# Kernel optimization log

Hardware: AMD Instinct MI355X
Metric: run time of the kernel (lower is better)

## Reference

```python
import jax, jax.numpy as jnp
import numpy as np
import math

H = 1024
E = 16
ENT_STRENGTH = 0.5
COHERENCE_TIME = 10.0
TIME_STEP = 0.0
K = 2
# static list of rotation pairs (i<j), applied sequentially as in the torch double loop
PAIRS = np.array([(i, j) for i in range(E) for j in range(i + 1, E)], dtype=np.int32)


def _mlp(x, w1, b1, w2, b2):
    h = jax.nn.gelu(x @ w1 + b1, approximate=False)  # torch default GELU = exact erf
    return h @ w2 + b2


def _apply_entanglement(amps, ent):
    # sequential Givens rotations over expert pairs; carry shape [B,S,E]
    pairs = jnp.asarray(PAIRS)

    def step(carry, pair):
        i, j = pair[0], pair[1]
        angle = ent[i, j] * ENT_STRENGTH
        c, s = jnp.cos(angle), jnp.sin(angle)
        ai = jnp.take(carry, i, axis=-1)  # [B,S]
        aj = jnp.take(carry, j, axis=-1)
        oh_i = jax.nn.one_hot(i, E, dtype=carry.dtype)
        oh_j = jax.nn.one_hot(j, E, dtype=carry.dtype)
        new = (carry * (1.0 - oh_i - oh_j)
               + (c * ai - s * aj)[..., None] * oh_i
               + (s * ai + c * aj)[..., None] * oh_j)
        return new, None

    out, _ = jax.lax.scan(step, amps, pairs)
    return out


def setup_inputs() -> dict:
    key = jax.random.key(0)
    ks = jax.random.split(key, 10)
    sc1 = 1.0 / math.sqrt(H)
    sc2 = 1.0 / math.sqrt(H // 2)
    return {
        "hidden_states": jax.random.normal(ks[0], (4, 4096, H), dtype=jnp.float32),
        "w1a": jax.random.uniform(ks[1], (H, H // 2), jnp.float32, -sc1, sc1),
        "b1a": jnp.zeros((H // 2,), jnp.float32),
        "w2a": jax.random.uniform(ks[2], (H // 2, E), jnp.float32, -sc2, sc2),
        "b2a": jnp.zeros((E,), jnp.float32),
        "w1p": jax.random.uniform(ks[3], (H, H // 2), jnp.float32, -sc1, sc1),
        "b1p": jnp.zeros((H // 2,), jnp.float32),
        "w2p": jax.random.uniform(ks[4], (H // 2, E), jnp.float32, -sc2, sc2),
        "b2p": jnp.zeros((E,), jnp.float32),
        "ent": jax.random.normal(ks[5], (E, E), dtype=jnp.float32) * 0.1,
    }


def reference(hidden_states, w1a, b1a, w2a, b2a, w1p, b1p, w2p, b2p, ent):
    raw_amps = _mlp(hidden_states, w1a, b1a, w2a, b2a)                 # [B,S,E]
    raw_phases = jnp.tanh(_mlp(hidden_states, w1p, b1p, w2p, b2p)) * jnp.float32(math.pi)
    amplitudes = jnp.sqrt(jax.nn.softmax(jnp.abs(raw_amps), axis=-1))
    entangled = _apply_entanglement(amplitudes, ent)
    coherence = jnp.exp(jnp.float32(-TIME_STEP / COHERENCE_TIME))      # time_step buffer = 0 -> 1.0
    decoherent = entangled * coherence
    probs = decoherent ** 2
    probs = probs / jnp.maximum(jnp.sum(jnp.abs(probs), axis=-1, keepdims=True), 1e-12)
    top_p, top_i = jax.lax.top_k(probs, K)
    top_p = top_p / jnp.maximum(jnp.sum(jnp.abs(top_p), axis=-1, keepdims=True), 1e-12)
    return top_p, top_i, decoherent, raw_phases, probs
```

## Files before the change

kernel.cpp:

```cpp
#include <hip/hip_runtime.h>
#include <math.h>

#define NTOK   16384
#define HDIM   1024
#define HHALF  512
#define NE     16

#define OFF_TP  0
#define OFF_TI  (NTOK * 2)
#define OFF_DEC (NTOK * 4)
#define OFF_PH  (OFF_DEC + NTOK * NE)
#define OFF_PR  (OFF_PH + NTOK * NE)

typedef _Float16 half8 __attribute__((ext_vector_type(8)));
typedef _Float16 half4 __attribute__((ext_vector_type(4)));
typedef float f32x16 __attribute__((ext_vector_type(16)));
typedef float f32x4 __attribute__((ext_vector_type(4)));

#define LO_SCALE     2048.0f
#define LO_SCALE_INV (1.0f / 2048.0f)
#define MFMA32(a,b,c) __builtin_amdgcn_mfma_f32_32x32x16_f16(a,b,c,0,0,0)
#define MFMA16(a,b,c) __builtin_amdgcn_mfma_f32_16x16x32_f16(a,b,c,0,0,0)

__device__ __forceinline__ float gelu_exact(float x) {
    return 0.5f * x * (1.0f + erff(x * 0.70710678118654752440f));
}

__device__ __forceinline__ void cvt_split(float4 v, half4& hi, half4& lo) {
    _Float16 h0 = (_Float16)v.x, h1 = (_Float16)v.y,
             h2 = (_Float16)v.z, h3 = (_Float16)v.w;
    hi = (half4){h0, h1, h2, h3};
    lo = (half4){(_Float16)((v.x - (float)h0) * LO_SCALE),
                 (_Float16)((v.y - (float)h1) * LO_SCALE),
                 (_Float16)((v.z - (float)h2) * LO_SCALE),
                 (_Float16)((v.w - (float)h3) * LO_SCALE)};
}

__global__ void __launch_bounds__(256)
qir_wtrans(const float* __restrict__ w1a, const float* __restrict__ w1p,
           _Float16* __restrict__ wt, float* __restrict__ out)
{
    int u = blockIdx.x * 256 + threadIdx.x;
    out[OFF_PH + u] = 0.0f;
    out[OFF_PH + 262144 + u] = 0.0f;

    int l  = u & 63;
    int f  = (u >> 6) & 7;
    int sl = (u >> 9) & 7;
    int kc = (u >> 12) & 31;
    int ph = u >> 17;
    int nf = f >> 2, kh = (f >> 1) & 1, pl = f & 1;
    int col = sl * 64 + nf * 32 + (l & 31);
    int k0  = kc * 32 + kh * 16 + (l >> 5) * 8;
    const float* __restrict__ W = ph ? w1p : w1a;
    half8 v;
    #pragma unroll
    for (int j = 0; j < 8; ++j) {
        float x = W[(size_t)(k0 + j) * HHALF + col];
        _Float16 h = (_Float16)x;
        v[j] = pl ? (_Float16)((x - (float)h) * LO_SCALE) : h;
    }
    *(half8*)&wt[(size_t)u * 8] = v;
}

__device__ __forceinline__ void kstep(
    int kc, const float* __restrict__ aptr, const _Float16* __restrict__ bptr,
    char* Acur, char* Anxt, int a_rd, int a_off0, int a_off1,
    half8 (&Bc)[8], half8 (&Bn)[8],
    float4 (&xw)[2], float4 (&xl)[2],
    f32x16& a00, f32x16& a01, f32x16& a10, f32x16& a11,
    f32x16& c00, f32x16& c01, f32x16& c10, f32x16& c11)
{
    if (kc + 2 < 32) {
        xl[0] = *(const float4*)(aptr + (kc + 2) * 32);
        xl[1] = *(const float4*)(aptr + (kc + 2) * 32 + 16);
    }
    if (kc + 1 < 32) {
        #pragma unroll
        for (int f = 0; f < 8; ++f)
            Bn[f] = *(const half8*)(bptr + (size_t)(kc + 1) * 32768 + f * 512);
    }
    #pragma unroll
    for (int kh = 0; kh < 2; ++kh) {
        const char* Ah = Acur + kh * 4096 + a_rd;
        half8 ah0 = *(const half8*)(Ah);
        half8 ah1 = *(const half8*)(Ah + 512);
        half8 al0 = *(const half8*)(Ah + 8192);
        half8 al1 = *(const half8*)(Ah + 8192 + 512);
        half8 bh0 = Bc[kh * 2],     bl0 = Bc[kh * 2 + 1];
        half8 bh1 = Bc[4 + kh * 2], bl1 = Bc[4 + kh * 2 + 1];
        a00 = MFMA32(ah0, bh0, a00); c00 = MFMA32(al0, bh0, c00); c00 = MFMA32(ah0, bl0, c00);
        a01 = MFMA32(ah0, bh1, a01); c01 = MFMA32(al0, bh1, c01); c01 = MFMA32(ah0, bl1, c01);
        a10 = MFMA32(ah1, bh0, a10); c10 = MFMA32(al1, bh0, c10); c10 = MFMA32(ah1, bl0, c10);
        a11 = MFMA32(ah1, bh1, a11); c11 = MFMA32(al1, bh1, c11); c11 = MFMA32(ah1, bl1, c11);
    }
    if (kc + 1 < 32) {
        half4 hv, lv;
        cvt_split(xw[0], hv, lv);
        *(half4*)(Anxt + a_off0) = hv; *(half4*)(Anxt + a_off0 + 8192) = lv;
        cvt_split(xw[1], hv, lv);
        *(half4*)(Anxt + a_off1) = hv; *(half4*)(Anxt + a_off1 + 8192) = lv;
    }
    __syncthreads();
}

__global__ void __launch_bounds__(512, 2)
qir_gemm(const float* __restrict__ xg, const _Float16* __restrict__ wt,
         const float* __restrict__ b1a, const float* __restrict__ w2a, const float* __restrict__ b2a,
         const float* __restrict__ b1p, const float* __restrict__ w2p, const float* __restrict__ b2p,
         float* __restrict__ out)
{
    extern __shared__ char smem[];
    const int tid = threadIdx.x;
    const int l  = tid & 63;
    const int w  = tid >> 6;
    const int wm = w >> 2;
    const int wn = w & 3;
    const int bid  = blockIdx.x;
    const int ph   = bid & 1;
    const int nh   = (bid >> 1) & 1;
    const int mblk = bid >> 2;
    const int tok0 = mblk * 128;

    const float* __restrict__ b1 = ph ? b1p : b1a;
    const float* __restrict__ w2 = ph ? w2p : w2a;
    const float* __restrict__ b2 = ph ? b2p : b2a;
    const _Float16* __restrict__ wtp = wt + ((size_t)ph << 20);

    char* const Ab0 = smem;
    char* const Ab1 = smem + 16384;

    const int r  = tid >> 2;
    const int kq = tid & 3;
    const float* __restrict__ aptr = xg + (size_t)(tok0 + r) * HDIM + kq * 4;
    const int a_off0 = (kq >> 1) * 2048 + r * 16 + (kq & 1) * 8;
    const int a_off1 = a_off0 + 4096;
    const int a_rd = (l >> 5) * 2048 + (wm * 64 + (l & 31)) * 16;

    const _Float16* __restrict__ bptr = wtp + (nh * 4 + wn) * 4096 + (size_t)l * 8;

    f32x16 a00{}, a01{}, a10{}, a11{}, c00{}, c01{}, c10{}, c11{};
    #pragma unroll
    for (int rg = 0; rg < 16; ++rg) {
        a00[rg] = 0.f; a01[rg] = 0.f; a10[rg] = 0.f; a11[rg] = 0.f;
        c00[rg] = 0.f; c01[rg] = 0.f; c10[rg] = 0.f; c11[rg] = 0.f;
    }

    half8 Bc[8], Bn[8];
    float4 xw[2], xl[2];

    {
        float4 v0 = *(const float4*)(aptr);
        float4 v1 = *(const float4*)(aptr + 16);
        half4 hv, lv;
        cvt_split(v0, hv, lv);
        *(half4*)(Ab0 + a_off0) = hv; *(half4*)(Ab0 + a_off0 + 8192) = lv;
        cvt_split(v1, hv, lv);
        *(half4*)(Ab0 + a_off1) = hv; *(half4*)(Ab0 + a_off1 + 8192) = lv;
    }
    #pragma unroll
    for (int f = 0; f < 8; ++f) Bc[f] = *(const half8*)(bptr + f * 512);
    xw[0] = *(const float4*)(aptr + 32);
    xw[1] = *(const float4*)(aptr + 48);
    __syncthreads();

    for (int kk = 0; kk < 16; ++kk) {
        kstep(2 * kk,     aptr, bptr, Ab0, Ab1, a_rd, a_off0, a_off1,
              Bc, Bn, xw, xl, a00, a01, a10, a11, c00, c01, c10, c11);
        kstep(2 * kk + 1, aptr, bptr, Ab1, Ab0, a_rd, a_off0, a_off1,
              Bn, Bc, xl, xw, a00, a01, a10, a11, c00, c01, c10, c11);
    }

    const int col0 = nh * 256 + wn * 64 + (l & 31);
    const float bb0 = b1[col0], bb1 = b1[col0 + 32];
    #pragma unroll
    for (int rg = 0; rg < 16; ++rg) {
        a00[rg] = gelu_exact(a00[rg] + c00[rg] * LO_SCALE_INV + bb0);
        a01[rg] = gelu_exact(a01[rg] + c01[rg] * LO_SCALE_INV + bb1);
        a10[rg] = gelu_exact(a10[rg] + c10[rg] * LO_SCALE_INV + bb0);
        a11[rg] = gelu_exact(a11[rg] + c11[rg] * LO_SCALE_INV + bb1);
    }

    char* const Hw = smem + w * 4096;
    char* const hb = Hw + ((l >> 3) & 3) * 1024 + (l & 7) * 2;
    float* const P = (float*)(smem + 32768);

    half8 w2h[2], w2l[2];
    #pragma unroll
    for (int nf = 0; nf < 2; ++nf) {
        #pragma unroll
        for (int j = 0; j < 8; ++j) {
            int kg = nh * 256 + wn * 64 + nf * 32 + (l >> 4) * 8 + j;
            float v = w2[(size_t)kg * NE + (l & 15)];
            _Float16 hh = (_Float16)v;
            w2h[nf][j] = hh;
            w2l[nf][j] = (_Float16)((v - (float)hh) * LO_SCALE);
        }
    }

    f32x4 acc2[4], acc2s[4];
    #pragma unroll
    for (int m16 = 0; m16 < 4; ++m16)
        #pragma unroll
        for (int rg = 0; rg < 4; ++rg) { acc2[m16][rg] = 0.f; acc2s[m16][rg] = 0.f; }

#define H2PASS(ACC0, ACC1, NF, PL)                                             \
    {                                                                          \
        _Pragma("unroll")                                                      \
        for (int rg = 0; rg < 16; ++rg) {                                      \
            int row0 = (rg & 3) + 8 * (rg >> 2) + 4 * (l >> 5);                \
            { float vv = ACC0[rg]; _Float16 hh = (_Float16)vv;                 \
              *(_Float16*)(hb + row0 * 16) =                                   \
                  (PL) ? (_Float16)(vv - (float)hh) : hh; }                    \
            { float vv = ACC1[rg]; _Float16 hh = (_Float16)vv;                 \
              *(_Float16*)(hb + (32 + row0) * 16) =                            \
                  (PL) ? (_Float16)(vv - (float)hh) : hh; }                    \
        }                                                                      \
        _Pragma("unroll")                                                      \
        for (int m16 = 0; m16 < 4; ++m16) {                                    \
            half8 a2 = *(const half8*)(Hw + (l >> 4) * 1024 +                  \
                                       (m16 * 16 + (l & 15)) * 16);            \
            acc2[m16] = MFMA16(a2, w2h[NF], acc2[m16]);                        \
            if (!(PL)) acc2s[m16] = MFMA16(a2, w2l[NF], acc2s[m16]);           \
        }                                                                      \
    }

    H2PASS(a00, a10, 0, 0)
    H2PASS(a01, a11, 1, 0)
    H2PASS(a00, a10, 0, 1)
    H2PASS(a01, a11, 1, 1)
#undef H2PASS

    #pragma unroll
    for (int m16 = 0; m16 < 4; ++m16)
        #pragma unroll
        for (int rg = 0; rg < 4; ++rg) {
            int row = m16 * 16 + ((l >> 4) << 2) + rg;
            P[w * 1024 + row * 16 + (l & 15)] =
                acc2[m16][rg] + acc2s[m16][rg] * LO_SCALE_INV;
        }
    __syncthreads();

    #pragma unroll
    for (int rep = 0; rep < 4; ++rep) {
        int oi = tid + rep * 512;
        int t = oi >> 4, e = oi & 15;
        int bw = (t >> 6) * 4, tl = t & 63;
        float sum = 0.5f * b2[e]
                  + P[(bw + 0) * 1024 + tl * 16 + e]
                  + P[(bw + 1) * 1024 + tl * 16 + e]
                  + P[(bw + 2) * 1024 + tl * 16 + e]
                  + P[(bw + 3) * 1024 + tl * 16 + e];
        atomicAdd(out + (ph ? OFF_PH : OFF_PR) + (size_t)(tok0 + t) * NE + e, sum);
    }
}

__global__ void __launch_bounds__(512)
qir_mlp(const float* __restrict__ xg,
        const float* __restrict__ w1a, const float* __restrict__ b1a,
        const float* __restrict__ w2a, const float* __restrict__ b2a,
        const float* __restrict__ w1p, const float* __restrict__ b1p,
        const float* __restrict__ w2p, const float* __restrict__ b2p,
        float* __restrict__ out)
{
    __shared__ float sh_w[16][HHALF];
    __shared__ float sh_x[16][68];

    const int tid  = threadIdx.x;
    const int cg   = tid & 63;
    const int tg   = tid >> 6;
    const int tok0 = blockIdx.x * 64;
    const int cA   = cg * 4;
    const int cB   = 256 + cg * 4;

    for (int phase = 0; phase < 2; ++phase) {
        const float* __restrict__ w1 = phase ? w1p : w1a;
        const float* __restrict__ b1 = phase ? b1p : b1a;
        const float* __restrict__ w2 = phase ? w2p : w2a;
        const float* __restrict__ b2 = phase ? b2p : b2a;

        float acc[8][8];
        #pragma unroll
        for (int t = 0; t < 8; ++t)
            #pragma unroll
            for (int c = 0; c < 8; ++c) acc[t][c] = 0.0f;

        float4 wreg[4];
        float4 xreg = make_float4(0.f, 0.f, 0.f, 0.f);

        auto load_chunk = [&](int kc) {
            #pragma unroll
            for (int p = 0; p < 4; ++p) {
                int f  = tid + p * 512;
                int k  = f >> 7;
                int c4 = (f & 127) << 2;
                wreg[p] = *(const float4*)&w1[(kc * 16 + k) * HHALF + c4];
            }
            if (tid < 256) {
                int t  = tid >> 2;
                int k4 = (tid & 3) << 2;
                xreg = *(const float4*)&xg[(size_t)(tok0 + t) * HDIM + kc * 16 + k4];
            }
        };

        load_chunk(0);
        for (int kc = 0; kc < HDIM / 16; ++kc) {
            __syncthreads();
            #pragma unroll
            for (int p = 0; p < 4; ++p) {
                int f  = tid + p * 512;
                int k  = f >> 7;
                int c4 = (f & 127) << 2;
                *(float4*)&sh_w[k][c4] = wreg[p];
            }
            if (tid < 256) {
                int t  = tid >> 2;
                int k4 = (tid & 3) << 2;
                sh_x[k4 + 0][t] = xreg.x;
                sh_x[k4 + 1][t] = xreg.y;
                sh_x[k4 + 2][t] = xreg.z;
                sh_x[k4 + 3][t] = xreg.w;
            }
            __syncthreads();
            if (kc + 1 < HDIM / 16) load_chunk(kc + 1);

            #pragma unroll 4
            for (int k = 0; k < 16; ++k) {
                float4 xa = *(const float4*)&sh_x[k][tg * 8];
                float4 xb = *(const float4*)&sh_x[k][tg * 8 + 4];
                float4 wa = *(const float4*)&sh_w[k][cA];
                float4 wb = *(const float4*)&sh_w[k][cB];
                float xs[8] = {xa.x, xa.y, xa.z, xa.w, xb.x, xb.y, xb.z, xb.w};
                float ws[8] = {wa.x, wa.y, wa.z, wa.w, wb.x, wb.y, wb.z, wb.w};
                #pragma unroll
                for (int t = 0; t < 8; ++t)
                    #pragma unroll
                    for (int c = 0; c < 8; ++c)
                        acc[t][c] = fmaf(xs[t], ws[c], acc[t][c]);
            }
        }

        {
            float4 bA4 = *(const float4*)&b1[cA];
            float4 bB4 = *(const float4*)&b1[cB];
            float bs[8] = {bA4.x, bA4.y, bA4.z, bA4.w, bB4.x, bB4.y, bB4.z, bB4.w};
            #pragma unroll
            for (int t = 0; t < 8; ++t)
                #pragma unroll
                for (int c = 0; c < 8; ++c)
                    acc[t][c] = gelu_exact(acc[t][c] + bs[c]);
        }

        for (int e = 0; e < NE; ++e) {
            float w2v[8];
            #pragma unroll
            for (int j = 0; j < 4; ++j) {
                w2v[j]     = w2[(cA + j) * NE + e];
                w2v[4 + j] = w2[(cB + j) * NE + e];
            }
            float bias2 = b2[e];
            #pragma unroll
            for (int t = 0; t < 8; ++t) {
                float s = 0.0f;
                #pragma unroll
                for (int j = 0; j < 8; ++j) s = fmaf(acc[t][j], w2v[j], s);
                #pragma unroll
                for (int off = 1; off < 64; off <<= 1)
                    s += __shfl_xor(s, off, 64);
                if (cg == 0) {
                    float raw   = s + bias2;
                    int   token = tok0 + tg * 8 + t;
                    out[(phase ? OFF_PH : OFF_PR) + (size_t)token * NE + e] = raw;
                }
            }
        }
    }
}

__global__ void __launch_bounds__(256)
qir_epilogue(const float* __restrict__ ent, float* __restrict__ out)
{
    __shared__ float sh_c[120], sh_s[120];
    const int tid = threadIdx.x;
    if (tid < 120) {
        int rem = tid, i = 0;
        while (rem >= 15 - i) { rem -= 15 - i; ++i; }
        int j = i + 1 + rem;
        float ang = ent[i * NE + j] * 0.5f;
        sh_c[tid] = cosf(ang);
        sh_s[tid] = sinf(ang);
    }
    __syncthreads();

    const int token = blockIdx.x * 256 + tid;

    #pragma unroll
    for (int q = 0; q < 4; ++q) {
        float4 v = *(const float4*)&out[OFF_PH + (size_t)token * NE + q * 4];
        v.x = tanhf(v.x) * 3.14159265358979323846f;
        v.y = tanhf(v.y) * 3.14159265358979323846f;
        v.z = tanhf(v.z) * 3.14159265358979323846f;
        v.w = tanhf(v.w) * 3.14159265358979323846f;
        *(float4*)&out[OFF_PH + (size_t)token * NE + q * 4] = v;
    }

    float a[16];
    #pragma unroll
    for (int q = 0; q < 4; ++q) {
        float4 v = *(const float4*)&out[OFF_PR + (size_t)token * NE + q * 4];
        a[q*4+0] = v.x; a[q*4+1] = v.y; a[q*4+2] = v.z; a[q*4+3] = v.w;
    }

    float m = fabsf(a[0]);
    #pragma unroll
    for (int e = 1; e < 16; ++e) m = fmaxf(m, fabsf(a[e]));
    float ssum = 0.0f;
    #pragma unroll
    for (int e = 0; e < 16; ++e) { a[e] = expf(fabsf(a[e]) - m); ssum += a[e]; }
    float inv = 1.0f / ssum;
    #pragma unroll
    for (int e = 0; e < 16; ++e) a[e] = sqrtf(a[e] * inv);

    {
        int p = 0;
        #pragma unroll
        for (int i = 0; i < 16; ++i) {
            #pragma unroll
            for (int j = i + 1; j < 16; ++j) {
                float c = sh_c[p], s = sh_s[p]; ++p;
                float ai = a[i], aj = a[j];
                a[i] = c * ai - s * aj;
                a[j] = s * ai + c * aj;
            }
        }
    }

    #pragma unroll
    for (int q = 0; q < 4; ++q)
        *(float4*)&out[OFF_DEC + (size_t)token * NE + q * 4] =
            make_float4(a[q*4], a[q*4+1], a[q*4+2], a[q*4+3]);

    float pr[16];
    float s2 = 0.0f;
    #pragma unroll
    for (int e = 0; e < 16; ++e) { pr[e] = a[e] * a[e]; s2 += pr[e]; }
    float inv2 = 1.0f / fmaxf(s2, 1e-12f);
    #pragma unroll
    for (int e = 0; e < 16; ++e) pr[e] *= inv2;
    #pragma unroll
    for (int q = 0; q < 4; ++q)
        *(float4*)&out[OFF_PR + (size_t)token * NE + q * 4] =
            make_float4(pr[q*4], pr[q*4+1], pr[q*4+2], pr[q*4+3]);

    float bv = pr[0]; int bi = 0;
    #pragma unroll
    for (int e = 1; e < 16; ++e) if (pr[e] > bv) { bv = pr[e]; bi = e; }
    float sv = -1.0f; int si = 0;
    #pragma unroll
    for (int e = 0; e < 16; ++e) if (e != bi && pr[e] > sv) { sv = pr[e]; si = e; }
    float ts = fmaxf(fabsf(bv) + fabsf(sv), 1e-12f);
    out[OFF_TP + (size_t)token * 2 + 0] = bv / ts;
    out[OFF_TP + (size_t)token * 2 + 1] = sv / ts;
    out[OFF_TI + (size_t)token * 2 + 0] = (float)bi;
    out[OFF_TI + (size_t)token * 2 + 1] = (float)si;
}

extern "C" void kernel_launch(void* const* d_in, const int* in_sizes, int n_in,
                              void* d_out, int out_size, void* d_ws, size_t ws_size,
                              hipStream_t stream) {
    const float* xg  = (const float*)d_in[0];
    const float* w1a = (const float*)d_in[1];
    const float* b1a = (const float*)d_in[2];
    const float* w2a = (const float*)d_in[3];
    const float* b2a = (const float*)d_in[4];
    const float* w1p = (const float*)d_in[5];
    const float* b1p = (const float*)d_in[6];
    const float* w2p = (const float*)d_in[7];
    const float* b2p = (const float*)d_in[8];
    const float* ent = (const float*)d_in[9];
    float* out = (float*)d_out;

    if (ws_size >= (size_t)4 * 1024 * 1024) {
        _Float16* wt = (_Float16*)d_ws;
        qir_wtrans<<<1024, 256, 0, stream>>>(w1a, w1p, wt, out);
        qir_gemm<<<512, 512, 65536, stream>>>(xg, wt, b1a, w2a, b2a,
                                              b1p, w2p, b2p, out);
    } else {
        qir_mlp<<<NTOK / 64, 512, 0, stream>>>(xg, w1a, b1a, w2a, b2a,
                                               w1p, b1p, w2p, b2p, out);
    }
    qir_epilogue<<<NTOK / 256, 256, 0, stream>>>(ent, out);
}
```

Baseline: 129.7 us.

## Swizzle LDS layouts, hoist LDS reads ahead of MFMAs, and remap block order

Applies XOR swizzles to the A-tile and hidden-activation LDS layouts so that reads and writes spread across banks. In the k-step, all LDS A fragments are loaded up front, the next tile's stores are issued before the MFMA chain, and the MFMAs run under raised wave priority. __syncthreads is replaced by a raw lgkmcnt wait plus s_barrier. The block index mapping now puts the token block in the low bits, so concurrently running blocks share weight columns rather than tokens. The hand-written barrier does not wait on outstanding global loads (vmcnt), and it relies on all LDS stores having been issued before it.

```diff
diff --git a/kernel.cpp b/kernel.cpp
--- a/kernel.cpp
+++ b/kernel.cpp
@@ -21,6 +21,8 @@
 #define LO_SCALE_INV (1.0f / 2048.0f)
 #define MFMA32(a,b,c) __builtin_amdgcn_mfma_f32_32x32x16_f16(a,b,c,0,0,0)
 #define MFMA16(a,b,c) __builtin_amdgcn_mfma_f32_16x16x32_f16(a,b,c,0,0,0)
+
+#define BAR() asm volatile("s_waitcnt lgkmcnt(0)\n\ts_barrier" ::: "memory")
 
 __device__ __forceinline__ float gelu_exact(float x) {
     return 0.5f * x * (1.0f + erff(x * 0.70710678118654752440f));
@@ -35,6 +37,8 @@
                  (_Float16)((v.z - (float)h2) * LO_SCALE),
                  (_Float16)((v.w - (float)h3) * LO_SCALE)};
 }
+
+__device__ __forceinline__ int aswz(int r) { return (r * 16) ^ ((r & 24) << 2); }
 
 __global__ void __launch_bounds__(256)
 qir_wtrans(const float* __restrict__ w1a, const float* __restrict__ w1p,
@@ -80,20 +84,18 @@
         for (int f = 0; f < 8; ++f)
             Bn[f] = *(const half8*)(bptr + (size_t)(kc + 1) * 32768 + f * 512);
     }
-    #pragma unroll
-    for (int kh = 0; kh < 2; ++kh) {
-        const char* Ah = Acur + kh * 4096 + a_rd;
-        half8 ah0 = *(const half8*)(Ah);
-        half8 ah1 = *(const half8*)(Ah + 512);
-        half8 al0 = *(const half8*)(Ah + 8192);
-        half8 al1 = *(const half8*)(Ah + 8192 + 512);
-        half8 bh0 = Bc[kh * 2],     bl0 = Bc[kh * 2 + 1];
-        half8 bh1 = Bc[4 + kh * 2], bl1 = Bc[4 + kh * 2 + 1];
-        a00 = MFMA32(ah0, bh0, a00); c00 = MFMA32(al0, bh0, c00); c00 = MFMA32(ah0, bl0, c00);
-        a01 = MFMA32(ah0, bh1, a01); c01 = MFMA32(al0, bh1, c01); c01 = MFMA32(ah0, bl1, c01);
-        a10 = MFMA32(ah1, bh0, a10); c10 = MFMA32(al1, bh0, c10); c10 = MFMA32(ah1, bl0, c10);
-        a11 = MFMA32(ah1, bh1, a11); c11 = MFMA32(al1, bh1, c11); c11 = MFMA32(ah1, bl1, c11);
-    }
+
+    const char* Ah0 = Acur + a_rd;
+    const char* Ah1 = Acur + 4096 + a_rd;
+    half8 ah0_0 = *(const half8*)(Ah0);
+    half8 ah1_0 = *(const half8*)(Ah0 + 512);
+    half8 al0_0 = *(const half8*)(Ah0 + 8192);
+    half8 al1_0 = *(const half8*)(Ah0 + 8192 + 512);
+    half8 ah0_1 = *(const half8*)(Ah1);
+    half8 ah1_1 = *(const half8*)(Ah1 + 512);
+    half8 al0_1 = *(const half8*)(Ah1 + 8192);
+    half8 al1_1 = *(const half8*)(Ah1 + 8192 + 512);
+
     if (kc + 1 < 32) {
         half4 hv, lv;
         cvt_split(xw[0], hv, lv);
@@ -101,7 +103,25 @@
         cvt_split(xw[1], hv, lv);
         *(half4*)(Anxt + a_off1) = hv; *(half4*)(Anxt + a_off1 + 8192) = lv;
     }
-    __syncthreads();
+
+    __builtin_amdgcn_s_setprio(1);
+    {
+        half8 bh0 = Bc[0], bl0 = Bc[1], bh1 = Bc[4], bl1 = Bc[5];
+        a00 = MFMA32(ah0_0, bh0, a00); c00 = MFMA32(al0_0, bh0, c00); c00 = MFMA32(ah0_0, bl0, c00);
+        a01 = MFMA32(ah0_0, bh1, a01); c01 = MFMA32(al0_0, bh1, c01); c01 = MFMA32(ah0_0, bl1, c01);
+        a10 = MFMA32(ah1_0, bh0, a10); c10 = MFMA32(al1_0, bh0, c10); c10 = MFMA32(ah1_0, bl0, c10);
+        a11 = MFMA32(ah1_0, bh1, a11); c11 = MFMA32(al1_0, bh1, c11); c11 = MFMA32(ah1_0, bl1, c11);
+    }
+    {
+        half8 bh0 = Bc[2], bl0 = Bc[3], bh1 = Bc[6], bl1 = Bc[7];
+        a00 = MFMA32(ah0_1, bh0, a00); c00 = MFMA32(al0_1, bh0, c00); c00 = MFMA32(ah0_1, bl0, c00);
+        a01 = MFMA32(ah0_1, bh1, a01); c01 = MFMA32(al0_1, bh1, c01); c01 = MFMA32(ah0_1, bl1, c01);
+        a10 = MFMA32(ah1_1, bh0, a10); c10 = MFMA32(al1_1, bh0, c10); c10 = MFMA32(ah1_1, bl0, c10);
+        a11 = MFMA32(ah1_1, bh1, a11); c11 = MFMA32(al1_1, bh1, c11); c11 = MFMA32(ah1_1, bl1, c11);
+    }
+    __builtin_amdgcn_s_setprio(0);
+
+    BAR();
 }
 
 __global__ void __launch_bounds__(512, 2)
@@ -117,9 +137,10 @@
     const int wm = w >> 2;
     const int wn = w & 3;
     const int bid  = blockIdx.x;
-    const int ph   = bid & 1;
-    const int nh   = (bid >> 1) & 1;
-    const int mblk = bid >> 2;
+    const int mblk = bid & 127;
+    const int v    = bid >> 7;
+    const int ph   = v & 1;
+    const int nh   = v >> 1;
     const int tok0 = mblk * 128;
 
     const float* __restrict__ b1 = ph ? b1p : b1a;
@@ -133,9 +154,9 @@
     const int r  = tid >> 2;
     const int kq = tid & 3;
     const float* __restrict__ aptr = xg + (size_t)(tok0 + r) * HDIM + kq * 4;
-    const int a_off0 = (kq >> 1) * 2048 + r * 16 + (kq & 1) * 8;
+    const int a_off0 = (kq >> 1) * 2048 + aswz(r) + (kq & 1) * 8;
     const int a_off1 = a_off0 + 4096;
-    const int a_rd = (l >> 5) * 2048 + (wm * 64 + (l & 31)) * 16;
+    const int a_rd = (l >> 5) * 2048 + aswz(wm * 64 + (l & 31));
 
     const _Float16* __restrict__ bptr = wtp + (nh * 4 + wn) * 4096 + (size_t)l * 8;
 
@@ -162,7 +183,7 @@
     for (int f = 0; f < 8; ++f) Bc[f] = *(const half8*)(bptr + f * 512);
     xw[0] = *(const float4*)(aptr + 32);
     xw[1] = *(const float4*)(aptr + 48);
-    __syncthreads();
+    BAR();
 
     for (int kk = 0; kk < 16; ++kk) {
         kstep(2 * kk,     aptr, bptr, Ab0, Ab1, a_rd, a_off0, a_off1,
@@ -182,7 +203,11 @@
     }
 
     char* const Hw = smem + w * 4096;
-    char* const hb = Hw + ((l >> 3) & 3) * 1024 + (l & 7) * 2;
+    const int hp   = (l >> 3) & 3;
+    char* const hb = Hw + hp * 1024 + (l & 7) * 2;
+    const int hxor = hp << 4;
+    const int rp   = l >> 4;
+    const int rxor = rp << 4;
     float* const P = (float*)(smem + 32768);
 
     half8 w2h[2], w2l[2];
@@ -191,10 +216,10 @@
         #pragma unroll
         for (int j = 0; j < 8; ++j) {
             int kg = nh * 256 + wn * 64 + nf * 32 + (l >> 4) * 8 + j;
-            float v = w2[(size_t)kg * NE + (l & 15)];
-            _Float16 hh = (_Float16)v;
+            float vv = w2[(size_t)kg * NE + (l & 15)];
+            _Float16 hh = (_Float16)vv;
             w2h[nf][j] = hh;
-            w2l[nf][j] = (_Float16)((v - (float)hh) * LO_SCALE);
+            w2l[nf][j] = (_Float16)((vv - (float)hh) * LO_SCALE);
         }
     }
 
@@ -210,16 +235,16 @@
         for (int rg = 0; rg < 16; ++rg) {                                      \
             int row0 = (rg & 3) + 8 * (rg >> 2) + 4 * (l >> 5);                \
             { float vv = ACC0[rg]; _Float16 hh = (_Float16)vv;                 \
-              *(_Float16*)(hb + row0 * 16) =                                   \
+              *(_Float16*)(hb + ((row0 * 16) ^ hxor)) =                        \
                   (PL) ? (_Float16)(vv - (float)hh) : hh; }                    \
             { float vv = ACC1[rg]; _Float16 hh = (_Float16)vv;                 \
-              *(_Float16*)(hb + (32 + row0) * 16) =                            \
+              *(_Float16*)(hb + (((32 + row0) * 16) ^ hxor)) =                 \
                   (PL) ? (_Float16)(vv - (float)hh) : hh; }                    \
         }                                                                      \
         _Pragma("unroll")                                                      \
         for (int m16 = 0; m16 < 4; ++m16) {                                    \
-            half8 a2 = *(const half8*)(Hw + (l >> 4) * 1024 +                  \
-                                       (m16 * 16 + (l & 15)) * 16);            \
+            half8 a2 = *(const half8*)(Hw + rp * 1024 +                        \
+                                       (((m16 * 16 + (l & 15)) * 16) ^ rxor)); \
             acc2[m16] = MFMA16(a2, w2h[NF], acc2[m16]);                        \
             if (!(PL)) acc2s[m16] = MFMA16(a2, w2l[NF], acc2s[m16]);           \
         }                                                                      \
```

Measured after the change: 154.6 us. 1.19x slower.
